# Kernel optimization log

Hardware: AMD Instinct MI355X
Metric: run time of the kernel (lower is better)

The kernel has to match this reference:

```python
import math
import jax, jax.numpy as jnp
import numpy as np

B, L, D, H, DFF, T, V = 512, 128, 128, 4, 256, 2048, 20000
LN_EPS = 1e-5
LOG_SIGMA0 = math.log(0.1)


def _keygen(base):
    c = [0]
    def nk():
        k = jax.random.fold_in(base, c[0]); c[0] += 1
        return k
    return nk


def bayes_linear(x, wmu, wls, bmu, bls, nk):
    # weight = mu + exp(log_sigma) * eps (fresh eps every call, as in BayesLinear.forward)
    w = wmu + jnp.exp(wls) * jax.random.normal(nk(), wmu.shape, wmu.dtype)
    b = bmu + jnp.exp(bls) * jax.random.normal(nk(), bmu.shape, bmu.dtype)
    return jnp.einsum('...d,od->...o', x, w) + b


def layer_norm(x, g, b):
    m = x.mean(-1, keepdims=True)
    v = ((x - m) ** 2).mean(-1, keepdims=True)
    return (x - m) / jnp.sqrt(v + LN_EPS) * g + b


def mha(q, k, v, wmu, wls, bmu, bls, nk):
    # wmu: [4, D, D] for q, k, v, o projections
    dk = D // H
    def proj(x, i):
        return bayes_linear(x, wmu[i], wls[i], bmu[i], bls[i], nk)
    def split(x):
        return x.reshape(B, L, H, dk).transpose(0, 2, 1, 3)
    Q, K, Vh = split(proj(q, 0)), split(proj(k, 1)), split(proj(v, 2))
    probs = jax.nn.softmax(jnp.einsum('bhqd,bhkd->bhqk', Q, K) / math.sqrt(dk), axis=-1)
    out = jnp.einsum('bhqk,bhkd->bhqd', probs, Vh).transpose(0, 2, 1, 3).reshape(B, L, D)
    return bayes_linear(out, wmu[3], wls[3], bmu[3], bls[3], nk)


def setup_inputs() -> dict:
    key = jax.random.key(0)
    ks = iter(jax.random.split(key, 64))
    def u(shape, fan_in):
        s = 1.0 / math.sqrt(fan_in)
        return jax.random.uniform(next(ks), shape, jnp.float32, -s, s)
    def ls(shape):
        return jnp.full(shape, LOG_SIGMA0, jnp.float32)
    return dict(
        event_set=jax.random.randint(next(ks), (B, L), 0, V),
        time=jax.random.uniform(next(ks), (B, L), jnp.float32),
        mask=jax.random.randint(next(ks), (B, L), 0, L),
        set_size=jax.random.randint(next(ks), (B,), 1, L),
        emb=jax.random.normal(next(ks), (V, D), jnp.float32),
        dec_wmu=u((2, 8, D, D), D), dec_wls=ls((2, 8, D, D)),
        dec_bmu=u((2, 8, D), D), dec_bls=ls((2, 8, D)),
        ffn1_wmu=u((2, DFF, D), D), ffn1_wls=ls((2, DFF, D)),
        ffn1_bmu=u((2, DFF), D), ffn1_bls=ls((2, DFF)),
        ffn2_wmu=u((2, D, DFF), DFF), ffn2_wls=ls((2, D, DFF)),
        ffn2_bmu=u((2, D), DFF), ffn2_bls=ls((2, D)),
        ln_g=jnp.ones((2, 3, D), jnp.float32), ln_b=jnp.zeros((2, 3, D), jnp.float32),
        alpha_wmu=u((5, T, D), D), alpha_wls=ls((5, T, D)),
        alpha_bmu=u((5, T), D), alpha_bls=ls((5, T)),
        at_wmu=u((5, 1, D), D), at_wls=ls((5, 1, D)),
        at_bmu=u((5, 1), D), at_bls=ls((5, 1)),
        em_w=u((5, T, D), D), em_b=u((5, T), D),
        es_w=u((5, T, D), D), es_b=u((5, T), D),
        tm_w=u((5, 1, D), D), tm_b=u((5, 1), D),
        ts_w=u((5, 1, D), D), ts_b=u((5, 1), D),
    )


def reference(event_set, time, mask, set_size, emb,
              dec_wmu, dec_wls, dec_bmu, dec_bls,
              ffn1_wmu, ffn1_wls, ffn1_bmu, ffn1_bls,
              ffn2_wmu, ffn2_wls, ffn2_bmu, ffn2_bls,
              ln_g, ln_b, alpha_wmu, alpha_wls, alpha_bmu, alpha_bls,
              at_wmu, at_wls, at_bmu, at_bls,
              em_w, em_b, es_w, es_b, tm_w, tm_b, ts_w, ts_b):
    nk = _keygen(jax.random.key(42))
    x = emb[event_set]                                     # [B, L, D]
    # sinusoidal positional encoding driven by `mask` (integer positions)
    pos = mask.astype(jnp.float32)
    div = jnp.exp(jnp.arange(D, dtype=jnp.float32) * (-math.log(10000.0) / D))
    ang = pos[..., None] * div                             # [B, L, D]
    pos_enc = jnp.where((mask % 2 == 0)[..., None], jnp.sin(ang), jnp.cos(ang))
    inp_x = x + pos_enc
    # two decoder layers: self-attn on x, cross-attn against inp_x (dropout = eval identity)
    for l in range(2):
        a = mha(x, x, x, dec_wmu[l, :4], dec_wls[l, :4], dec_bmu[l, :4], dec_bls[l, :4], nk)
        x = layer_norm(x + a, ln_g[l, 0], ln_b[l, 0])
        a = mha(x, inp_x, inp_x, dec_wmu[l, 4:], dec_wls[l, 4:], dec_bmu[l, 4:], dec_bls[l, 4:], nk)
        x = layer_norm(x + a, ln_g[l, 1], ln_b[l, 1])
        h1 = jax.nn.relu(bayes_linear(x, ffn1_wmu[l], ffn1_wls[l], ffn1_bmu[l], ffn1_bls[l], nk))
        f = bayes_linear(h1, ffn2_wmu[l], ffn2_wls[l], ffn2_bmu[l], ffn2_bls[l], nk)
        x = layer_norm(x + f, ln_g[l, 2], ln_b[l, 2])
    h = x[:, 0, :]                                          # [B, D]
    # 5 Bayesian alpha heads -> softmax over mixture dim (vectorized over k)
    aw = alpha_wmu + jnp.exp(alpha_wls) * jax.random.normal(nk(), alpha_wmu.shape)
    ab = alpha_bmu + jnp.exp(alpha_bls) * jax.random.normal(nk(), alpha_bmu.shape)
    alpha = jax.nn.softmax(jnp.einsum('bd,ktd->btk', h, aw) + ab.T[None], axis=2)   # [B, T, 5]
    atw = at_wmu + jnp.exp(at_wls) * jax.random.normal(nk(), at_wmu.shape)
    atb = at_bmu + jnp.exp(at_bls) * jax.random.normal(nk(), at_bmu.shape)
    alpha_t = jax.nn.softmax(jnp.einsum('bd,kd->bk', h, atw[:, 0]) + atb[:, 0][None], axis=1)  # [B, 5]
    # mixture of 5 reparameterized Gaussian predictors (plain Linears)
    means = jnp.einsum('bd,ktd->bkt', h, em_w) + em_b[None]          # [B, 5, T]
    stds = jnp.exp(jnp.einsum('bd,ktd->bkt', h, es_w) + es_b[None])
    noise_e = jax.random.normal(nk(), (B, 5, T))
    event_pred = jnp.sum(jnp.swapaxes(alpha, 1, 2) * (means + stds * noise_e), axis=1)   # [B, T]
    tmeans = jnp.einsum('bd,kd->bk', h, tm_w[:, 0]) + tm_b[:, 0][None]                   # [B, 5]
    tstds = jnp.exp(jnp.einsum('bd,kd->bk', h, ts_w[:, 0]) + ts_b[:, 0][None])
    noise_t = jax.random.normal(nk(), (B, 5))
    time_pred = jnp.sum(alpha_t * (tmeans + tstds * noise_t), axis=1, keepdims=True)     # [B, 1]
    return event_pred, time_pred
```

## Files before the change

### kernel.cpp

```cpp
#include <hip/hip_runtime.h>
#include <cstdint>
#include <cstddef>


#define NB   512
#define NL   128
#define ND   128
#define NH   4
#define NDFF 256
#define NT   2048
#define BL   (NB * NL)

typedef __attribute__((ext_vector_type(8))) short bf16x8;
typedef __attribute__((ext_vector_type(4))) float f32x4;

#define MFMA16(a, b, c) __builtin_amdgcn_mfma_f32_16x16x32_bf16((a), (b), (c), 0, 0, 0)

__host__ __device__ __forceinline__ void tf2x32(uint32_t k0, uint32_t k1,
                                                uint32_t x0, uint32_t x1,
                                                uint32_t& o0, uint32_t& o1)
{
  const uint32_t ks2 = k0 ^ k1 ^ 0x1BD11BDAu;
  x0 += k0; x1 += k1;
#define TF_RND(r) { x0 += x1; x1 = (x1 << (r)) | (x1 >> (32 - (r))); x1 ^= x0; }
  TF_RND(13) TF_RND(15) TF_RND(26) TF_RND(6)
  x0 += k1;  x1 += ks2 + 1u;
  TF_RND(17) TF_RND(29) TF_RND(16) TF_RND(24)
  x0 += ks2; x1 += k0 + 2u;
  TF_RND(13) TF_RND(15) TF_RND(26) TF_RND(6)
  x0 += k0;  x1 += k1 + 3u;
  TF_RND(17) TF_RND(29) TF_RND(16) TF_RND(24)
  x0 += k1;  x1 += ks2 + 4u;
  TF_RND(13) TF_RND(15) TF_RND(26) TF_RND(6)
  x0 += ks2; x1 += k0 + 5u;
#undef TF_RND
  o0 = x0; o1 = x1;
}

__device__ __forceinline__ float erfinv32(float x)
{
  float w = -log1pf(-__fmul_rn(x, x));
  float p;
  if (w < 5.0f) {
    w = w - 2.5f;
    p = 2.81022636e-08f;
    p = __fadd_rn( 3.43273939e-07f, __fmul_rn(p, w));
    p = __fadd_rn(-3.5233877e-06f,  __fmul_rn(p, w));
    p = __fadd_rn(-4.39150654e-06f, __fmul_rn(p, w));
    p = __fadd_rn( 0.00021858087f,  __fmul_rn(p, w));
    p = __fadd_rn(-0.00125372503f,  __fmul_rn(p, w));
    p = __fadd_rn(-0.00417768164f,  __fmul_rn(p, w));
    p = __fadd_rn( 0.246640727f,    __fmul_rn(p, w));
    p = __fadd_rn( 1.50140941f,     __fmul_rn(p, w));
  } else {
    w = sqrtf(w) - 3.0f;
    p = -0.000200214257f;
    p = __fadd_rn( 0.000100950558f, __fmul_rn(p, w));
    p = __fadd_rn( 0.00134934322f,  __fmul_rn(p, w));
    p = __fadd_rn(-0.00367342844f,  __fmul_rn(p, w));
    p = __fadd_rn( 0.00573950773f,  __fmul_rn(p, w));
    p = __fadd_rn(-0.0076224613f,   __fmul_rn(p, w));
    p = __fadd_rn( 0.00943887047f,  __fmul_rn(p, w));
    p = __fadd_rn( 1.00167406f,     __fmul_rn(p, w));
    p = __fadd_rn( 2.83297682f,     __fmul_rn(p, w));
  }
  return __fmul_rn(p, x);
}

__device__ __forceinline__ float bits_to_normal(uint32_t bits)
{
  const float lo = -0.99999994f;
  float f = __uint_as_float((bits >> 9) | 0x3F800000u) - 1.0f;
  float u = __fadd_rn(__fmul_rn(f, 2.0f), lo);
  u = fmaxf(lo, u);
  return __fmul_rn(1.41421356f, erfinv32(u));
}

__device__ __forceinline__ float jax_normal_idx(uint32_t k0, uint32_t k1, uint32_t idx)
{
  uint32_t o0, o1;
  tf2x32(k0, k1, 0u, idx, o0, o1);
  return bits_to_normal(o0 ^ o1);
}

__device__ __forceinline__ ushort f2bf(float f)
{
  uint32_t u = __float_as_uint(f);
  u += 0x7fffu + ((u >> 16) & 1u);
  return (ushort)(u >> 16);
}

__device__ __forceinline__ int pk128(int row, int col)
{
  return (((row >> 4) * 4 + (col >> 5)) * 64 + ((col >> 3) & 3) * 16 + (row & 15)) * 8
         + (col & 7);
}
__device__ __forceinline__ int pk_w2(int row, int col)
{
  return (col >> 7) * 16384 +
         (((row >> 4) * 4 + ((col >> 5) & 3)) * 64 + ((col >> 3) & 3) * 16 + (row & 15)) * 8
         + (col & 7);
}

#define SA_DECB 262144
#define SA_F1W  264192
#define SA_F1B  329728
#define SA_F2W  330240
#define SA_F2B  395776
#define SA_AW   396032
#define SA_AB   1706752
#define SA_ATW  1716992
#define SA_ATB  1717632
#define SA_TOT  1717637

#define BW_DEC  0
#define BW_F1   262144
#define BW_F2   327680
#define BW_AW   393216
#define BW_TOT  1703936

#define BF_DECB 0
#define BF_F1B  2048
#define BF_F2B  2560
#define BF_AB   2816
#define BF_ATW  13056
#define BF_ATB  13696
#define BF_TOT  13701

__global__ __launch_bounds__(256) void sample_all_kernel(
    const float* __restrict__ dec_wmu, const float* __restrict__ dec_wls,
    const float* __restrict__ dec_bmu, const float* __restrict__ dec_bls,
    const float* __restrict__ f1_wmu,  const float* __restrict__ f1_wls,
    const float* __restrict__ f1_bmu,  const float* __restrict__ f1_bls,
    const float* __restrict__ f2_wmu,  const float* __restrict__ f2_wls,
    const float* __restrict__ f2_bmu,  const float* __restrict__ f2_bls,
    const float* __restrict__ a_wmu,   const float* __restrict__ a_wls,
    const float* __restrict__ a_bmu,   const float* __restrict__ a_bls,
    const float* __restrict__ at_wmu,  const float* __restrict__ at_wls,
    const float* __restrict__ at_bmu,  const float* __restrict__ at_bls,
    ushort* __restrict__ wbf, float* __restrict__ wf32)
{
  const int i = blockIdx.x * 256 + threadIdx.x;
  if (i >= SA_TOT) return;
  const float* mu; const float* ls;
  uint32_t c, idx;
  int bf_dst = -1, f32_dst = -1;
  if (i < SA_DECB) {
    int s = i >> 14, t = i & 16383;
    mu = dec_wmu + i; ls = dec_wls + i;
    c = 2u * s + (s >= 8 ? 4u : 0u); idx = (uint32_t)t;
    bf_dst = BW_DEC + s * 16384 + pk128(t >> 7, t & 127);
  } else if (i < SA_F1W) {
    int t = i - SA_DECB; int s = t >> 7;
    mu = dec_bmu + t; ls = dec_bls + t;
    c = 2u * s + 1u + (s >= 8 ? 4u : 0u); idx = (uint32_t)(t & 127);
    f32_dst = BF_DECB + t;
  } else if (i < SA_F1B) {
    int t = i - SA_F1W; int s = t >> 15, tl = t & 32767;
    mu = f1_wmu + t; ls = f1_wls + t;
    c = 16u + 20u * s; idx = (uint32_t)tl;
    bf_dst = BW_F1 + s * 32768 + pk128(tl >> 7, tl & 127);
  } else if (i < SA_F2W) {
    int t = i - SA_F1B; int s = t >> 8;
    mu = f1_bmu + t; ls = f1_bls + t;
    c = 17u + 20u * s; idx = (uint32_t)(t & 255);
    f32_dst = BF_F1B + t;
  } else if (i < SA_F2B) {
    int t = i - SA_F2W; int s = t >> 15, tl = t & 32767;
    mu = f2_wmu + t; ls = f2_wls + t;
    c = 18u + 20u * s; idx = (uint32_t)tl;
    bf_dst = BW_F2 + s * 32768 + pk_w2(tl >> 8, tl & 255);
  } else if (i < SA_AW) {
    int t = i - SA_F2B; int s = t >> 7;
    mu = f2_bmu + t; ls = f2_bls + t;
    c = 19u + 20u * s; idx = (uint32_t)(t & 127);
    f32_dst = BF_F2B + t;
  } else if (i < SA_AB) {
    int t = i - SA_AW;
    mu = a_wmu + t; ls = a_wls + t; c = 40u; idx = (uint32_t)t;
    int kcomp = t >> 18, rem = t & 262143;
    bf_dst = BW_AW + pk128(kcomp * 2048 + (rem >> 7), rem & 127);
  } else if (i < SA_ATW) {
    int t = i - SA_AB;
    mu = a_bmu + t; ls = a_bls + t; c = 41u; idx = (uint32_t)t;
    f32_dst = BF_AB + t;
  } else if (i < SA_ATB) {
    int t = i - SA_ATW;
    mu = at_wmu + t; ls = at_wls + t; c = 42u; idx = (uint32_t)t;
    f32_dst = BF_ATW + t;
  } else {
    int t = i - SA_ATB;
    mu = at_bmu + t; ls = at_bls + t; c = 43u; idx = (uint32_t)t;
    f32_dst = BF_ATB + t;
  }
  uint32_t k0, k1;
  tf2x32(0u, 42u, 0u, c, k0, k1);
  float v = mu[0] + expf(ls[0]) * jax_normal_idx(k0, k1, idx);
  if (bf_dst >= 0) wbf[bf_dst] = f2bf(v);
  else             wf32[f32_dst] = v;
}

__global__ __launch_bounds__(256) void pack_head_kernel(
    const float* __restrict__ em_w, const float* __restrict__ es_w,
    ushort* __restrict__ EMp, ushort* __restrict__ ESp)
{
  int i = blockIdx.x * 256 + threadIdx.x;
  int kcomp = i >> 18, rem = i & 262143;
  int dst = pk128(kcomp * 2048 + (rem >> 7), rem & 127);
  EMp[dst] = f2bf(em_w[i]);
  ESp[dst] = f2bf(es_w[i]);
}

#define STR 136

__global__ __launch_bounds__(512, 1) void decoder_mega_kernel(
    const int* __restrict__ ev, const int* __restrict__ mask,
    const float* __restrict__ emb,
    const ushort* __restrict__ WBF, const float* __restrict__ WF32,
    const float* __restrict__ lng_all, const float* __restrict__ lnb_all,
    float* __restrict__ Xh, ushort* __restrict__ Hb)
{
  __shared__ ushort WL[16384];
  __shared__ ushort Kt[128][STR];
  __shared__ ushort Vt[128][STR];
  __shared__ ushort Xb[128][STR];

  const int b = blockIdx.x;
  const int tid = threadIdx.x;
  const int w = tid >> 6, l = tid & 63;
  const int g = l >> 4, r16 = l & 15;
  const f32x4 zero = {0.f, 0.f, 0.f, 0.f};
  ushort* KtLin = &Kt[0][0];

  auto stageW = [&](ushort* dst, const ushort* src) {
#pragma unroll
    for (int it = 0; it < 4; ++it) {
      __builtin_amdgcn_global_load_lds(
          (const uint32_t*)(src + (size_t)(it * 512 + tid) * 8),
          (uint32_t*)(dst + (it * 512 + w * 64) * 8), 16, 0, 0);
    }
  };
  auto wfrag = [&](const ushort* WB, int fid) -> bf16x8 {
    return *(const bf16x8*)(WB + (size_t)((fid << 6) + l) * 8);
  };

  float xreg[8][4];
  {
    int ecr[4];
#pragma unroll
    for (int r = 0; r < 4; ++r) ecr[r] = ev[b * NL + 16 * w + 4 * g + r];
#pragma unroll
    for (int c = 0; c < 8; ++c)
#pragma unroll
      for (int r = 0; r < 4; ++r) {
        float x = emb[(size_t)ecr[r] * ND + 16 * c + r16];
        xreg[c][r] = x;
        Xb[16 * w + 4 * g + r][16 * c + r16] = f2bf(x);
      }
  }
  bf16x8 inpx[4];
  {
    const int row = 16 * w + r16;
    const int ea = ev[b * NL + row];
    const int mk = mask[b * NL + row];
    const bool even = (mk & 1) == 0;
    const float fm = (float)mk;
#pragma unroll
    for (int ks = 0; ks < 4; ++ks) {
      float4 x0 = *(const float4*)(emb + (size_t)ea * ND + 32 * ks + 8 * g);
      float4 x1 = *(const float4*)(emb + (size_t)ea * ND + 32 * ks + 8 * g + 4);
      float xs[8] = {x0.x, x0.y, x0.z, x0.w, x1.x, x1.y, x1.z, x1.w};
      bf16x8 v;
#pragma unroll
      for (int e = 0; e < 8; ++e) {
        int d = 32 * ks + 8 * g + e;
        float div = expf((float)d * (float)(-9.210340371976184 / 128.0));
        float ang = fm * div;
        float pe = even ? sinf(ang) : cosf(ang);
        v[e] = (short)f2bf(xs[e] + pe);
      }
      inpx[ks] = v;
    }
  }

#pragma unroll 1
  for (int st = 0; st < 6; ++st) {
    const int lay = st / 3, m = st - 3 * lay;
    const float* lng = lng_all + (size_t)(lay * 3 + m) * ND;
    const float* lnb = lnb_all + (size_t)(lay * 3 + m) * ND;
    f32x4 acc2[8];
#pragma unroll
    for (int c = 0; c < 8; ++c) acc2[c] = zero;
    float bo[8];

    if (m < 2) {
      const int s0 = lay * 8 + m * 4;
      const ushort* W4 = WBF + BW_DEC + (size_t)s0 * 16384;
      const float*  B4 = WF32 + BF_DECB + (size_t)s0 * 128;

      __syncthreads();
      stageW(KtLin, W4 + 16384);
      stageW(WL,    W4 + 2 * 16384);
      __syncthreads();

      f32x4 kacc[8], vacc[8];
#pragma unroll
      for (int c = 0; c < 8; ++c) { kacc[c] = zero; vacc[c] = zero; }
#pragma unroll
      for (int ks = 0; ks < 4; ++ks) {
        bf16x8 a = (m == 0) ? *(const bf16x8*)&Xb[16 * w + r16][32 * ks + 8 * g]
                            : inpx[ks];
#pragma unroll
        for (int c = 0; c < 8; ++c) {
          kacc[c] = MFMA16(a, wfrag(KtLin, 4 * c + ks), kacc[c]);
          vacc[c] = MFMA16(a, wfrag(WL,    4 * c + ks), vacc[c]);
        }
      }
      __syncthreads();

#pragma unroll
      for (int c = 0; c < 8; ++c) {
        float kb = B4[128 + 16 * c + r16];
#pragma unroll
        for (int r = 0; r < 4; ++r)
          Kt[16 * w + 4 * g + r][16 * c + r16] = f2bf(kacc[c][r] + kb);
        float vb = B4[256 + 16 * c + r16];
        ushort4 pkv;
        pkv.x = f2bf(vacc[c][0] + vb); pkv.y = f2bf(vacc[c][1] + vb);
        pkv.z = f2bf(vacc[c][2] + vb); pkv.w = f2bf(vacc[c][3] + vb);
        *(ushort4*)&Vt[16 * c + r16][16 * w + 4 * g] = pkv;
      }
      stageW(WL, W4);
      __syncthreads();

      {
        f32x4 qacc[8];
#pragma unroll
        for (int c = 0; c < 8; ++c) qacc[c] = zero;
#pragma unroll
        for (int ks = 0; ks < 4; ++ks) {
          bf16x8 a = *(const bf16x8*)&Xb[16 * w + r16][32 * ks + 8 * g];
#pragma unroll
          for (int c = 0; c < 8; ++c)
            qacc[c] = MFMA16(a, wfrag(WL, 4 * c + ks), qacc[c]);
        }
#pragma unroll
        for (int c = 0; c < 8; ++c) {
          float qb = B4[16 * c + r16];
#pragma unroll
          for (int r = 0; r < 4; ++r)
            Xb[16 * w + 4 * g + r][16 * c + r16] = f2bf(qacc[c][r] + qb);
        }
      }
      __syncthreads();

      ushort (*Ps)[72] = (ushort(*)[72])WL;
      const float scale = 0.1767766952966369f;
      f32x4 oacc[4][2];
#pragma unroll
      for (int h = 0; h < 4; ++h) { oacc[h][0] = zero; oacc[h][1] = zero; }
#pragma unroll 1
      for (int h = 0; h < 4; ++h) {
        bf16x8 qa = *(const bf16x8*)&Xb[16 * w + r16][32 * h + 8 * g];
        f32x4 s[8];
#pragma unroll
        for (int c = 0; c < 8; ++c) {
          bf16x8 kv = *(const bf16x8*)&Kt[16 * c + r16][32 * h + 8 * g];
          s[c] = MFMA16(qa, kv, zero);
        }
        float pv[4][8];
#pragma unroll
        for (int r = 0; r < 4; ++r) {
          float v[8]; float mx = -1e30f;
#pragma unroll
          for (int c = 0; c < 8; ++c) { v[c] = s[c][r] * scale; mx = fmaxf(mx, v[c]); }
#pragma unroll
          for (int o = 1; o < 16; o <<= 1) mx = fmaxf(mx, __shfl_xor(mx, o));
          float sum = 0.f;
#pragma unroll
          for (int c = 0; c < 8; ++c) { v[c] = __expf(v[c] - mx); sum += v[c]; }
#pragma unroll
          for (int o = 1; o < 16; o <<= 1) sum += __shfl_xor(sum, o);
          float inv = 1.0f / sum;
#pragma unroll
          for (int c = 0; c < 8; ++c) pv[r][c] = v[c] * inv;
        }
#pragma unroll
        for (int kc = 0; kc < 4; ++kc) {
          const int po = (kc & 1) * 32;
#pragma unroll
          for (int c2 = 0; c2 < 2; ++c2)
#pragma unroll
            for (int r = 0; r < 4; ++r)
              Ps[16 * w + 4 * g + r][po + 16 * c2 + r16] = f2bf(pv[r][2 * kc + c2]);
          bf16x8 pa = *(const bf16x8*)&Ps[16 * w + r16][po + 8 * g];
#pragma unroll
          for (int cc = 0; cc < 2; ++cc) {
            bf16x8 vv = *(const bf16x8*)&Vt[32 * h + 16 * cc + r16][32 * kc + 8 * g];
            oacc[h][cc] = MFMA16(pa, vv, oacc[h][cc]);
          }
        }
      }
      __syncthreads();

#pragma unroll
      for (int h = 0; h < 4; ++h)
#pragma unroll
        for (int cc = 0; cc < 2; ++cc)
#pragma unroll
          for (int r = 0; r < 4; ++r)
            Kt[16 * w + 4 * g + r][32 * h + 16 * cc + r16] = f2bf(oacc[h][cc][r]);
      stageW(WL, W4 + 3 * 16384);
      __syncthreads();
#pragma unroll
      for (int ks = 0; ks < 4; ++ks) {
        bf16x8 a = *(const bf16x8*)&Kt[16 * w + r16][32 * ks + 8 * g];
#pragma unroll
        for (int c = 0; c < 8; ++c)
          acc2[c] = MFMA16(a, wfrag(WL, 4 * c + ks), acc2[c]);
      }
#pragma unroll
      for (int c = 0; c < 8; ++c) bo[c] = B4[384 + 16 * c + r16];
    } else {
      const ushort* W1p = WBF + BW_F1 + (size_t)lay * 32768;
      const ushort* W2p = WBF + BW_F2 + (size_t)lay * 32768;
      const float*  B1 = WF32 + BF_F1B + (size_t)lay * 256;
      const float*  B2 = WF32 + BF_F2B + (size_t)lay * 128;

      __syncthreads();
      stageW(WL,    W1p);
      stageW(KtLin, W1p + 16384);
      __syncthreads();

      f32x4 acc1[16];
#pragma unroll
      for (int c = 0; c < 16; ++c) acc1[c] = zero;
#pragma unroll
      for (int ks = 0; ks < 4; ++ks) {
        bf16x8 a = *(const bf16x8*)&Xb[16 * w + r16][32 * ks + 8 * g];
#pragma unroll
        for (int c = 0; c < 8; ++c) {
          acc1[c]     = MFMA16(a, wfrag(WL,    4 * c + ks), acc1[c]);
          acc1[8 + c] = MFMA16(a, wfrag(KtLin, 4 * c + ks), acc1[8 + c]);
        }
      }
      __syncthreads();

#pragma unroll
      for (int c = 0; c < 16; ++c) {
        float bb = B1[16 * c + r16];
#pragma unroll
        for (int r = 0; r < 4; ++r) {
          float o = fmaxf(acc1[c][r] + bb, 0.f);
          if (c < 8) Vt[16 * w + 4 * g + r][16 * c + r16] = f2bf(o);
          else       Kt[16 * w + 4 * g + r][16 * (c - 8) + r16] = f2bf(o);
        }
      }
      stageW(WL, W2p);
      __syncthreads();
#pragma unroll
      for (int kl = 0; kl < 4; ++kl) {
        bf16x8 a = *(const bf16x8*)&Vt[16 * w + r16][32 * kl + 8 * g];
#pragma unroll
        for (int c = 0; c < 8; ++c)
          acc2[c] = MFMA16(a, wfrag(WL, 4 * c + kl), acc2[c]);
      }
      __syncthreads();
      stageW(WL, W2p + 16384);
      __syncthreads();
#pragma unroll
      for (int kl = 0; kl < 4; ++kl) {
        bf16x8 a = *(const bf16x8*)&Kt[16 * w + r16][32 * kl + 8 * g];
#pragma unroll
        for (int c = 0; c < 8; ++c)
          acc2[c] = MFMA16(a, wfrag(WL, 4 * c + kl), acc2[c]);
      }
#pragma unroll
      for (int c = 0; c < 8; ++c) bo[c] = B2[16 * c + r16];
    }

    float gg[8], lb[8];
#pragma unroll
    for (int c = 0; c < 8; ++c) { gg[c] = lng[16 * c + r16]; lb[c] = lnb[16 * c + r16]; }
#pragma unroll
    for (int r = 0; r < 4; ++r) {
      float xv[8];
#pragma unroll
      for (int c = 0; c < 8; ++c) xv[c] = acc2[c][r] + bo[c] + xreg[c][r];
      float s = 0.f;
#pragma unroll
      for (int c = 0; c < 8; ++c) s += xv[c];
#pragma unroll
      for (int o = 1; o < 16; o <<= 1) s += __shfl_xor(s, o);
      float mean = s * (1.0f / 128.0f);
      float q = 0.f;
#pragma unroll
      for (int c = 0; c < 8; ++c) { float d = xv[c] - mean; q += d * d; }
#pragma unroll
      for (int o = 1; o < 16; o <<= 1) q += __shfl_xor(q, o);
      float inv = 1.0f / sqrtf(q * (1.0f / 128.0f) + 1e-5f);
#pragma unroll
      for (int c = 0; c < 8; ++c) {
        float o = (xv[c] - mean) * inv * gg[c] + lb[c];
        xreg[c][r] = o;
        Xb[16 * w + 4 * g + r][16 * c + r16] = f2bf(o);
      }
    }
  }

  if (w == 0 && g == 0) {
#pragma unroll
    for (int c = 0; c < 8; ++c) {
      Xh[(size_t)b * ND + 16 * c + r16] = xreg[c][0];
      Hb[(size_t)b * ND + 16 * c + r16] = f2bf(xreg[c][0]);
    }
  }
}

__global__ __launch_bounds__(256) void head_fused_kernel(
    const ushort* __restrict__ Hb,
    const ushort* __restrict__ AWp, const float* __restrict__ ABs,
    const ushort* __restrict__ EMp, const float* __restrict__ em_b,
    const ushort* __restrict__ ESp, const float* __restrict__ es_b,
    float* __restrict__ out, uint32_t k0, uint32_t k1)
{
  const int tt = blockIdx.x;
  const int t0 = tt * 16;
  const int bm = blockIdx.y * 128;
  const int tid = threadIdx.x;
  const int w = tid >> 6, l = tid & 63;
  const int g = l >> 4, r16 = l & 15;
  const f32x4 zero = {0.f, 0.f, 0.f, 0.f};
  const int tl = t0 + r16;

  f32x4 aA[2][5], aE[2][5], aS[2][5];
#pragma unroll
  for (int t = 0; t < 2; ++t)
#pragma unroll
    for (int k = 0; k < 5; ++k) { aA[t][k] = zero; aE[t][k] = zero; aS[t][k] = zero; }

#pragma unroll
  for (int ks = 0; ks < 4; ++ks) {
    bf16x8 a0 = *(const bf16x8*)(Hb + (size_t)(bm + 32 * w + r16) * 128 + 32 * ks + 8 * g);
    bf16x8 a1 = *(const bf16x8*)(Hb + (size_t)(bm + 32 * w + 16 + r16) * 128 + 32 * ks + 8 * g);
#pragma unroll
    for (int k = 0; k < 5; ++k) {
      const size_t CB = (((size_t)(k * 128 + tt) * 4 + ks) * 64 + l) * 8;
      bf16x8 wa = *(const bf16x8*)(AWp + CB);
      aA[0][k] = MFMA16(a0, wa, aA[0][k]);
      aA[1][k] = MFMA16(a1, wa, aA[1][k]);
      bf16x8 we = *(const bf16x8*)(EMp + CB);
      aE[0][k] = MFMA16(a0, we, aE[0][k]);
      aE[1][k] = MFMA16(a1, we, aE[1][k]);
      bf16x8 wsv = *(const bf16x8*)(ESp + CB);
      aS[0][k] = MFMA16(a0, wsv, aS[0][k]);
      aS[1][k] = MFMA16(a1, wsv, aS[1][k]);
    }
  }

  float bA[5], bE[5], bS[5];
#pragma unroll
  for (int k = 0; k < 5; ++k) {
    bA[k] = ABs[k * NT + tl];
    bE[k] = em_b[k * NT + tl];
    bS[k] = es_b[k * NT + tl];
  }

#pragma unroll
  for (int t = 0; t < 2; ++t)
#pragma unroll
    for (int r = 0; r < 4; ++r) {
      const int brow = bm + 32 * w + 16 * t + 4 * g + r;
      float lg[5];
      float mx = -1e30f;
#pragma unroll
      for (int k = 0; k < 5; ++k) { lg[k] = aA[t][k][r] + bA[k]; mx = fmaxf(mx, lg[k]); }
      float se = 0.f;
#pragma unroll
      for (int k = 0; k < 5; ++k) { lg[k] = expf(lg[k] - mx); se += lg[k]; }
      const float inv = 1.0f / se;
      float acc = 0.f;
#pragma unroll
      for (int k = 0; k < 5; ++k) {
        float nz = jax_normal_idx(k0, k1, (uint32_t)((brow * 5 + k) * NT + tl));
        float mean = aE[t][k][r] + bE[k];
        float sd   = expf(aS[t][k][r] + bS[k]);
        acc += (lg[k] * inv) * (mean + sd * nz);
      }
      out[(size_t)brow * NT + tl] = acc;
    }
}

__global__ __launch_bounds__(64) void time_head_kernel(
    const float* __restrict__ Xh, const float* __restrict__ atw,
    const float* __restrict__ atb, const float* __restrict__ tmw,
    const float* __restrict__ tmb, const float* __restrict__ tsw,
    const float* __restrict__ tsb, float* __restrict__ out,
    uint32_t k0, uint32_t k1)
{
  const int b = blockIdx.x;
  const int l = threadIdx.x;
  const float* h = Xh + (size_t)b * ND;
  const float h0 = h[l], h1 = h[l + 64];
  float lg[5], tm[5], tsl[5];
#pragma unroll
  for (int k = 0; k < 5; ++k) {
    float s0 = fmaf(h0, atw[k * ND + l], h1 * atw[k * ND + l + 64]);
    float s1 = fmaf(h0, tmw[k * ND + l], h1 * tmw[k * ND + l + 64]);
    float s2 = fmaf(h0, tsw[k * ND + l], h1 * tsw[k * ND + l + 64]);
#pragma unroll
    for (int o = 32; o; o >>= 1) {
      s0 += __shfl_xor(s0, o);
      s1 += __shfl_xor(s1, o);
      s2 += __shfl_xor(s2, o);
    }
    lg[k] = s0 + atb[k]; tm[k] = s1 + tmb[k]; tsl[k] = s2 + tsb[k];
  }
  if (l == 0) {
    float mx = lg[0];
    for (int k = 1; k < 5; ++k) mx = fmaxf(mx, lg[k]);
    float se = 0.f;
    for (int k = 0; k < 5; ++k) { lg[k] = expf(lg[k] - mx); se += lg[k]; }
    float acc = 0.f;
    for (int k = 0; k < 5; ++k) {
      float nz = jax_normal_idx(k0, k1, (uint32_t)(b * 5 + k));
      acc += (lg[k] / se) * (tm[k] + expf(tsl[k]) * nz);
    }
    out[b] = acc;
  }
}

extern "C" void kernel_launch(void* const* d_in, const int* in_sizes, int n_in,
                              void* d_out, int out_size, void* d_ws, size_t ws_size,
                              hipStream_t stream)
{
  (void)in_sizes; (void)n_in; (void)out_size; (void)ws_size;

  const int*   ev      = (const int*)d_in[0];
  const int*   mask    = (const int*)d_in[2];
  const float* emb     = (const float*)d_in[4];
  const float* dec_wmu = (const float*)d_in[5];
  const float* dec_wls = (const float*)d_in[6];
  const float* dec_bmu = (const float*)d_in[7];
  const float* dec_bls = (const float*)d_in[8];
  const float* f1_wmu  = (const float*)d_in[9];
  const float* f1_wls  = (const float*)d_in[10];
  const float* f1_bmu  = (const float*)d_in[11];
  const float* f1_bls  = (const float*)d_in[12];
  const float* f2_wmu  = (const float*)d_in[13];
  const float* f2_wls  = (const float*)d_in[14];
  const float* f2_bmu  = (const float*)d_in[15];
  const float* f2_bls  = (const float*)d_in[16];
  const float* ln_g    = (const float*)d_in[17];
  const float* ln_b    = (const float*)d_in[18];
  const float* a_wmu   = (const float*)d_in[19];
  const float* a_wls   = (const float*)d_in[20];
  const float* a_bmu   = (const float*)d_in[21];
  const float* a_bls   = (const float*)d_in[22];
  const float* at_wmu  = (const float*)d_in[23];
  const float* at_wls  = (const float*)d_in[24];
  const float* at_bmu  = (const float*)d_in[25];
  const float* at_bls  = (const float*)d_in[26];
  const float* em_w    = (const float*)d_in[27];
  const float* em_b    = (const float*)d_in[28];
  const float* es_w    = (const float*)d_in[29];
  const float* es_b    = (const float*)d_in[30];
  const float* tm_w    = (const float*)d_in[31];
  const float* tm_b    = (const float*)d_in[32];
  const float* ts_w    = (const float*)d_in[33];
  const float* ts_b    = (const float*)d_in[34];

  float* ws = (float*)d_ws;
  ushort* WBF  = (ushort*)ws;
  float*  WF32 = ws + BW_TOT / 2;
  ushort* EMp  = (ushort*)(WF32 + BF_TOT + 3);
  ushort* ESp  = EMp + 5 * NT * ND;
  ushort* Hb   = ESp + 5 * NT * ND;
  float*  Xh   = (float*)(Hb + (size_t)NB * ND);

  uint32_t fk0[46], fk1[46];
  for (uint32_t c = 0; c < 46; ++c) tf2x32(0u, 42u, 0u, c, fk0[c], fk1[c]);

  sample_all_kernel<<<dim3((SA_TOT + 255) / 256), dim3(256), 0, stream>>>(
      dec_wmu, dec_wls, dec_bmu, dec_bls,
      f1_wmu, f1_wls, f1_bmu, f1_bls,
      f2_wmu, f2_wls, f2_bmu, f2_bls,
      a_wmu, a_wls, a_bmu, a_bls,
      at_wmu, at_wls, at_bmu, at_bls, WBF, WF32);

  pack_head_kernel<<<dim3((5 * NT * ND) / 256), dim3(256), 0, stream>>>(
      em_w, es_w, EMp, ESp);

  decoder_mega_kernel<<<dim3(NB), dim3(512), 0, stream>>>(
      ev, mask, emb, WBF, WF32, ln_g, ln_b, Xh, Hb);

  float* out = (float*)d_out;
  head_fused_kernel<<<dim3(NT / 16, 4), dim3(256), 0, stream>>>(
      Hb, WBF + BW_AW, WF32 + BF_AB, EMp, em_b, ESp, es_b,
      out, fk0[44], fk1[44]);
  time_head_kernel<<<dim3(NB), dim3(64), 0, stream>>>(
      Xh, WF32 + BF_ATW, WF32 + BF_ATB, tm_w, tm_b, ts_w, ts_b,
      out + (size_t)NB * NT, fk0[45], fk1[45]);
}
```

Measured before the change: 328.6 us.

## Read weight fragments directly from global memory instead of staging into LDS

Drops the LDS weight buffer and the async global-to-LDS staging of each 128x128 weight matrix. MFMA B-fragments are now loaded straight from global memory, which is expected to be served mostly from L2. The Q projection is fused into the K/V projection loop, and many __syncthreads barriers tied to staging are removed. The intent is to cut barrier stalls and serialized staging phases, at the cost of each wave fetching the full weights on its own, raising L2 traffic and exposing global-load latency right next to the MFMAs.

Result: slower. 583.5 us (+77.6%).

```diff
diff --git a/kernel.cpp b/kernel.cpp
--- a/kernel.cpp
+++ b/kernel.cpp
@@ -220,28 +220,19 @@
     const float* __restrict__ lng_all, const float* __restrict__ lnb_all,
     float* __restrict__ Xh, ushort* __restrict__ Hb)
 {
-  __shared__ ushort WL[16384];
   __shared__ ushort Kt[128][STR];
   __shared__ ushort Vt[128][STR];
   __shared__ ushort Xb[128][STR];
+  __shared__ ushort Ps[128][72];
 
   const int b = blockIdx.x;
   const int tid = threadIdx.x;
   const int w = tid >> 6, l = tid & 63;
   const int g = l >> 4, r16 = l & 15;
   const f32x4 zero = {0.f, 0.f, 0.f, 0.f};
-  ushort* KtLin = &Kt[0][0];
-
-  auto stageW = [&](ushort* dst, const ushort* src) {
-#pragma unroll
-    for (int it = 0; it < 4; ++it) {
-      __builtin_amdgcn_global_load_lds(
-          (const uint32_t*)(src + (size_t)(it * 512 + tid) * 8),
-          (uint32_t*)(dst + (it * 512 + w * 64) * 8), 16, 0, 0);
-    }
-  };
-  auto wfrag = [&](const ushort* WB, int fid) -> bf16x8 {
-    return *(const bf16x8*)(WB + (size_t)((fid << 6) + l) * 8);
+
+  auto wfragG = [&](const ushort* Wp, int fid) -> bf16x8 {
+    return *(const bf16x8*)(Wp + ((size_t)(fid << 6) + l) * 8);
   };
 
   float xreg[8][4];
@@ -295,25 +286,24 @@
 
     if (m < 2) {
       const int s0 = lay * 8 + m * 4;
-      const ushort* W4 = WBF + BW_DEC + (size_t)s0 * 16384;
+      const ushort* Wq = WBF + BW_DEC + (size_t)s0 * 16384;
+      const ushort* Wk = Wq + 16384;
+      const ushort* Wv = Wq + 2 * 16384;
+      const ushort* Wo = Wq + 3 * 16384;
       const float*  B4 = WF32 + BF_DECB + (size_t)s0 * 128;
 
-      __syncthreads();
-      stageW(KtLin, W4 + 16384);
-      stageW(WL,    W4 + 2 * 16384);
-      __syncthreads();
-
-      f32x4 kacc[8], vacc[8];
-#pragma unroll
-      for (int c = 0; c < 8; ++c) { kacc[c] = zero; vacc[c] = zero; }
+      f32x4 qacc[8], kacc[8], vacc[8];
+#pragma unroll
+      for (int c = 0; c < 8; ++c) { qacc[c] = zero; kacc[c] = zero; vacc[c] = zero; }
 #pragma unroll
       for (int ks = 0; ks < 4; ++ks) {
-        bf16x8 a = (m == 0) ? *(const bf16x8*)&Xb[16 * w + r16][32 * ks + 8 * g]
-                            : inpx[ks];
+        bf16x8 ax = *(const bf16x8*)&Xb[16 * w + r16][32 * ks + 8 * g];
+        bf16x8 akv = (m == 0) ? ax : inpx[ks];
 #pragma unroll
         for (int c = 0; c < 8; ++c) {
-          kacc[c] = MFMA16(a, wfrag(KtLin, 4 * c + ks), kacc[c]);
-          vacc[c] = MFMA16(a, wfrag(WL,    4 * c + ks), vacc[c]);
+          qacc[c] = MFMA16(ax,  wfragG(Wq, 4 * c + ks), qacc[c]);
+          kacc[c] = MFMA16(akv, wfragG(Wk, 4 * c + ks), kacc[c]);
+          vacc[c] = MFMA16(akv, wfragG(Wv, 4 * c + ks), vacc[c]);
         }
       }
       __syncthreads();
@@ -329,32 +319,13 @@
         pkv.x = f2bf(vacc[c][0] + vb); pkv.y = f2bf(vacc[c][1] + vb);
         pkv.z = f2bf(vacc[c][2] + vb); pkv.w = f2bf(vacc[c][3] + vb);
         *(ushort4*)&Vt[16 * c + r16][16 * w + 4 * g] = pkv;
-      }
-      stageW(WL, W4);
+        float qb = B4[16 * c + r16];
+#pragma unroll
+        for (int r = 0; r < 4; ++r)
+          Xb[16 * w + 4 * g + r][16 * c + r16] = f2bf(qacc[c][r] + qb);
+      }
       __syncthreads();
 
-      {
-        f32x4 qacc[8];
-#pragma unroll
-        for (int c = 0; c < 8; ++c) qacc[c] = zero;
-#pragma unroll
-        for (int ks = 0; ks < 4; ++ks) {
-          bf16x8 a = *(const bf16x8*)&Xb[16 * w + r16][32 * ks + 8 * g];
-#pragma unroll
-          for (int c = 0; c < 8; ++c)
-            qacc[c] = MFMA16(a, wfrag(WL, 4 * c + ks), qacc[c]);
-        }
-#pragma unroll
-        for (int c = 0; c < 8; ++c) {
-          float qb = B4[16 * c + r16];
-#pragma unroll
-          for (int r = 0; r < 4; ++r)
-            Xb[16 * w + 4 * g + r][16 * c + r16] = f2bf(qacc[c][r] + qb);
-        }
-      }
-      __syncthreads();
-
-      ushort (*Ps)[72] = (ushort(*)[72])WL;
       const float scale = 0.1767766952966369f;
       f32x4 oacc[4][2];
 #pragma unroll
@@ -410,14 +381,12 @@
 #pragma unroll
           for (int r = 0; r < 4; ++r)
             Kt[16 * w + 4 * g + r][32 * h + 16 * cc + r16] = f2bf(oacc[h][cc][r]);
-      stageW(WL, W4 + 3 * 16384);
-      __syncthreads();
 #pragma unroll
       for (int ks = 0; ks < 4; ++ks) {
         bf16x8 a = *(const bf16x8*)&Kt[16 * w + r16][32 * ks + 8 * g];
 #pragma unroll
         for (int c = 0; c < 8; ++c)
-          acc2[c] = MFMA16(a, wfrag(WL, 4 * c + ks), acc2[c]);
+          acc2[c] = MFMA16(a, wfragG(Wo, 4 * c + ks), acc2[c]);
       }
 #pragma unroll
       for (int c = 0; c < 8; ++c) bo[c] = B4[384 + 16 * c + r16];
@@ -427,11 +396,6 @@
       const float*  B1 = WF32 + BF_F1B + (size_t)lay * 256;
       const float*  B2 = WF32 + BF_F2B + (size_t)lay * 128;
 
-      __syncthreads();
-      stageW(WL,    W1p);
-      stageW(KtLin, W1p + 16384);
-      __syncthreads();
-
       f32x4 acc1[16];
 #pragma unroll
       for (int c = 0; c < 16; ++c) acc1[c] = zero;
@@ -440,12 +404,10 @@
         bf16x8 a = *(const bf16x8*)&Xb[16 * w + r16][32 * ks + 8 * g];
 #pragma unroll
         for (int c = 0; c < 8; ++c) {
-          acc1[c]     = MFMA16(a, wfrag(WL,    4 * c + ks), acc1[c]);
-          acc1[8 + c] = MFMA16(a, wfrag(KtLin, 4 * c + ks), acc1[8 + c]);
+          acc1[c]     = MFMA16(a, wfragG(W1p,         4 * c + ks), acc1[c]);
+          acc1[8 + c] = MFMA16(a, wfragG(W1p + 16384, 4 * c + ks), acc1[8 + c]);
         }
       }
-      __syncthreads();
-
 #pragma unroll
       for (int c = 0; c < 16; ++c) {
         float bb = B1[16 * c + r16];
@@ -456,24 +418,19 @@
           else       Kt[16 * w + 4 * g + r][16 * (c - 8) + r16] = f2bf(o);
         }
       }
-      stageW(WL, W2p);
-      __syncthreads();
 #pragma unroll
       for (int kl = 0; kl < 4; ++kl) {
         bf16x8 a = *(const bf16x8*)&Vt[16 * w + r16][32 * kl + 8 * g];
 #pragma unroll
         for (int c = 0; c < 8; ++c)
-          acc2[c] = MFMA16(a, wfrag(WL, 4 * c + kl), acc2[c]);
-      }
-      __syncthreads();
-      stageW(WL, W2p + 16384);
-      __syncthreads();
+          acc2[c] = MFMA16(a, wfragG(W2p, 4 * c + kl), acc2[c]);
+      }
 #pragma unroll
       for (int kl = 0; kl < 4; ++kl) {
         bf16x8 a = *(const bf16x8*)&Kt[16 * w + r16][32 * kl + 8 * g];
 #pragma unroll
         for (int c = 0; c < 8; ++c)
-          acc2[c] = MFMA16(a, wfrag(WL, 4 * c + kl), acc2[c]);
+          acc2[c] = MFMA16(a, wfragG(W2p + 16384, 4 * c + kl), acc2[c]);
       }
 #pragma unroll
       for (int c = 0; c < 8; ++c) bo[c] = B2[16 * c + r16];
```

## Double-buffer decoder weight staging and swizzle LDS activation tiles

Applied to the files above, without the earlier changes.

The decoder megakernel gains a second LDS weight buffer. Each weight matrix's async global-to-LDS load is issued one GEMM ahead, including the first weight of the next sublayer, so weight fetches overlap with MFMA work instead of sitting between barriers. The padded activation tiles (stride 136) are replaced by unpadded 128-wide tiles with an XOR chunk swizzle to avoid bank conflicts. The head loop is also fully unrolled. LDS use grows, and the prefetch ordering relies on barriers that clear before the buffers are reused.

Result: slower. 343.8 us (+4.6%).

```diff
diff --git a/kernel.cpp b/kernel.cpp
--- a/kernel.cpp
+++ b/kernel.cpp
@@ -100,6 +100,15 @@
   return (col >> 7) * 16384 +
          (((row >> 4) * 4 + ((col >> 5) & 3)) * 64 + ((col >> 3) & 3) * 16 + (row & 15)) * 8
          + (col & 7);
+}
+
+__device__ __forceinline__ int swzc(int row, int chunk)
+{
+  return row * 128 + ((chunk ^ (row & 15)) << 3);
+}
+__device__ __forceinline__ int swz(int row, int col)
+{
+  return row * 128 + ((((col >> 3) ^ (row & 15)) << 3) | (col & 7));
 }
 
 #define SA_DECB 262144
@@ -211,8 +220,6 @@
   ESp[dst] = f2bf(es_w[i]);
 }
 
-#define STR 136
-
 __global__ __launch_bounds__(512, 1) void decoder_mega_kernel(
     const int* __restrict__ ev, const int* __restrict__ mask,
     const float* __restrict__ emb,
@@ -220,17 +227,17 @@
     const float* __restrict__ lng_all, const float* __restrict__ lnb_all,
     float* __restrict__ Xh, ushort* __restrict__ Hb)
 {
-  __shared__ ushort WL[16384];
-  __shared__ ushort Kt[128][STR];
-  __shared__ ushort Vt[128][STR];
-  __shared__ ushort Xb[128][STR];
+  __shared__ ushort WAu[16384];
+  __shared__ ushort WBu[16384];
+  __shared__ ushort KtU[16384];
+  __shared__ ushort VtU[16384];
+  __shared__ ushort XbU[16384];
 
   const int b = blockIdx.x;
   const int tid = threadIdx.x;
   const int w = tid >> 6, l = tid & 63;
   const int g = l >> 4, r16 = l & 15;
   const f32x4 zero = {0.f, 0.f, 0.f, 0.f};
-  ushort* KtLin = &Kt[0][0];
 
   auto stageW = [&](ushort* dst, const ushort* src) {
 #pragma unroll
@@ -240,9 +247,19 @@
           (uint32_t*)(dst + (it * 512 + w * 64) * 8), 16, 0, 0);
     }
   };
-  auto wfrag = [&](const ushort* WB, int fid) -> bf16x8 {
-    return *(const bf16x8*)(WB + (size_t)((fid << 6) + l) * 8);
+  auto wfrag = [&](const ushort* WBp, int fid) -> bf16x8 {
+    return *(const bf16x8*)(WBp + (size_t)((fid << 6) + l) * 8);
   };
+
+  const ushort* firstW[6];
+  firstW[0] = WBF + BW_DEC + (size_t)1 * 16384;
+  firstW[1] = WBF + BW_DEC + (size_t)5 * 16384;
+  firstW[2] = WBF + BW_F1;
+  firstW[3] = WBF + BW_DEC + (size_t)9 * 16384;
+  firstW[4] = WBF + BW_DEC + (size_t)13 * 16384;
+  firstW[5] = WBF + BW_F1 + 32768;
+
+  stageW(WAu, firstW[0]);
 
   float xreg[8][4];
   {
@@ -255,7 +272,7 @@
       for (int r = 0; r < 4; ++r) {
         float x = emb[(size_t)ecr[r] * ND + 16 * c + r16];
         xreg[c][r] = x;
-        Xb[16 * w + 4 * g + r][16 * c + r16] = f2bf(x);
+        XbU[swz(16 * w + 4 * g + r, 16 * c + r16)] = f2bf(x);
       }
   }
   bf16x8 inpx[4];
@@ -295,77 +312,91 @@
 
     if (m < 2) {
       const int s0 = lay * 8 + m * 4;
-      const ushort* W4 = WBF + BW_DEC + (size_t)s0 * 16384;
+      const ushort* Wq = WBF + BW_DEC + (size_t)(s0 + 0) * 16384;
+      const ushort* Wv = WBF + BW_DEC + (size_t)(s0 + 2) * 16384;
+      const ushort* Wo = WBF + BW_DEC + (size_t)(s0 + 3) * 16384;
       const float*  B4 = WF32 + BF_DECB + (size_t)s0 * 128;
 
       __syncthreads();
-      stageW(KtLin, W4 + 16384);
-      stageW(WL,    W4 + 2 * 16384);
-      __syncthreads();
-
-      f32x4 kacc[8], vacc[8];
-#pragma unroll
-      for (int c = 0; c < 8; ++c) { kacc[c] = zero; vacc[c] = zero; }
+      stageW(WBu, Wv);
+      f32x4 kacc[8];
+#pragma unroll
+      for (int c = 0; c < 8; ++c) kacc[c] = zero;
 #pragma unroll
       for (int ks = 0; ks < 4; ++ks) {
-        bf16x8 a = (m == 0) ? *(const bf16x8*)&Xb[16 * w + r16][32 * ks + 8 * g]
+        bf16x8 a = (m == 0) ? *(const bf16x8*)&XbU[swzc(16 * w + r16, 4 * ks + g)]
                             : inpx[ks];
 #pragma unroll
-        for (int c = 0; c < 8; ++c) {
-          kacc[c] = MFMA16(a, wfrag(KtLin, 4 * c + ks), kacc[c]);
-          vacc[c] = MFMA16(a, wfrag(WL,    4 * c + ks), vacc[c]);
-        }
-      }
-      __syncthreads();
-
+        for (int c = 0; c < 8; ++c)
+          kacc[c] = MFMA16(a, wfrag(WAu, 4 * c + ks), kacc[c]);
+      }
+
+      __syncthreads();
+      stageW(WAu, Wq);
 #pragma unroll
       for (int c = 0; c < 8; ++c) {
         float kb = B4[128 + 16 * c + r16];
 #pragma unroll
         for (int r = 0; r < 4; ++r)
-          Kt[16 * w + 4 * g + r][16 * c + r16] = f2bf(kacc[c][r] + kb);
-        float vb = B4[256 + 16 * c + r16];
-        ushort4 pkv;
-        pkv.x = f2bf(vacc[c][0] + vb); pkv.y = f2bf(vacc[c][1] + vb);
-        pkv.z = f2bf(vacc[c][2] + vb); pkv.w = f2bf(vacc[c][3] + vb);
-        *(ushort4*)&Vt[16 * c + r16][16 * w + 4 * g] = pkv;
-      }
-      stageW(WL, W4);
-      __syncthreads();
-
+          KtU[swz(16 * w + 4 * g + r, 16 * c + r16)] = f2bf(kacc[c][r] + kb);
+      }
+      {
+        f32x4 vacc[8];
+#pragma unroll
+        for (int c = 0; c < 8; ++c) vacc[c] = zero;
+#pragma unroll
+        for (int ks = 0; ks < 4; ++ks) {
+          bf16x8 a = (m == 0) ? *(const bf16x8*)&XbU[swzc(16 * w + r16, 4 * ks + g)]
+                              : inpx[ks];
+#pragma unroll
+          for (int c = 0; c < 8; ++c)
+            vacc[c] = MFMA16(a, wfrag(WBu, 4 * c + ks), vacc[c]);
+        }
+#pragma unroll
+        for (int c = 0; c < 8; ++c) {
+          float vb = B4[256 + 16 * c + r16];
+          ushort4 pkv;
+          pkv.x = f2bf(vacc[c][0] + vb); pkv.y = f2bf(vacc[c][1] + vb);
+          pkv.z = f2bf(vacc[c][2] + vb); pkv.w = f2bf(vacc[c][3] + vb);
+          *(ushort4*)&VtU[swzc(16 * c + r16, 2 * w + (g >> 1)) + (g & 1) * 4] = pkv;
+        }
+      }
+
+      __syncthreads();
+      stageW(WBu, Wo);
       {
         f32x4 qacc[8];
 #pragma unroll
         for (int c = 0; c < 8; ++c) qacc[c] = zero;
 #pragma unroll
         for (int ks = 0; ks < 4; ++ks) {
-          bf16x8 a = *(const bf16x8*)&Xb[16 * w + r16][32 * ks + 8 * g];
+          bf16x8 a = *(const bf16x8*)&XbU[swzc(16 * w + r16, 4 * ks + g)];
 #pragma unroll
           for (int c = 0; c < 8; ++c)
-            qacc[c] = MFMA16(a, wfrag(WL, 4 * c + ks), qacc[c]);
+            qacc[c] = MFMA16(a, wfrag(WAu, 4 * c + ks), qacc[c]);
         }
 #pragma unroll
         for (int c = 0; c < 8; ++c) {
           float qb = B4[16 * c + r16];
 #pragma unroll
           for (int r = 0; r < 4; ++r)
-            Xb[16 * w + 4 * g + r][16 * c + r16] = f2bf(qacc[c][r] + qb);
-        }
-      }
-      __syncthreads();
-
-      ushort (*Ps)[72] = (ushort(*)[72])WL;
+            XbU[swz(16 * w + 4 * g + r, 16 * c + r16)] = f2bf(qacc[c][r] + qb);
+        }
+      }
+
+      __syncthreads();
+      ushort (*Ps)[72] = (ushort(*)[72])WAu;
       const float scale = 0.1767766952966369f;
       f32x4 oacc[4][2];
 #pragma unroll
       for (int h = 0; h < 4; ++h) { oacc[h][0] = zero; oacc[h][1] = zero; }
-#pragma unroll 1
+#pragma unroll
       for (int h = 0; h < 4; ++h) {
-        bf16x8 qa = *(const bf16x8*)&Xb[16 * w + r16][32 * h + 8 * g];
+        bf16x8 qa = *(const bf16x8*)&XbU[swzc(16 * w + r16, 4 * h + g)];
         f32x4 s[8];
 #pragma unroll
         for (int c = 0; c < 8; ++c) {
-          bf16x8 kv = *(const bf16x8*)&Kt[16 * c + r16][32 * h + 8 * g];
+          bf16x8 kv = *(const bf16x8*)&KtU[swzc(16 * c + r16, 4 * h + g)];
           s[c] = MFMA16(qa, kv, zero);
         }
         float pv[4][8];
@@ -396,28 +427,27 @@
           bf16x8 pa = *(const bf16x8*)&Ps[16 * w + r16][po + 8 * g];
 #pragma unroll
           for (int cc = 0; cc < 2; ++cc) {
-            bf16x8 vv = *(const bf16x8*)&Vt[32 * h + 16 * cc + r16][32 * kc + 8 * g];
+            bf16x8 vv = *(const bf16x8*)&VtU[swzc(32 * h + 16 * cc + r16, 4 * kc + g)];
             oacc[h][cc] = MFMA16(pa, vv, oacc[h][cc]);
           }
         }
       }
-      __syncthreads();
-
+
+      __syncthreads();
+      if (st < 5) stageW(WAu, firstW[st + 1]);
 #pragma unroll
       for (int h = 0; h < 4; ++h)
 #pragma unroll
         for (int cc = 0; cc < 2; ++cc)
 #pragma unroll
           for (int r = 0; r < 4; ++r)
-            Kt[16 * w + 4 * g + r][32 * h + 16 * cc + r16] = f2bf(oacc[h][cc][r]);
-      stageW(WL, W4 + 3 * 16384);
-      __syncthreads();
+            KtU[swz(16 * w + 4 * g + r, 32 * h + 16 * cc + r16)] = f2bf(oacc[h][cc][r]);
 #pragma unroll
       for (int ks = 0; ks < 4; ++ks) {
-        bf16x8 a = *(const bf16x8*)&Kt[16 * w + r16][32 * ks + 8 * g];
+        bf16x8 a = *(const bf16x8*)&KtU[swzc(16 * w + r16, 4 * ks + g)];
 #pragma unroll
         for (int c = 0; c < 8; ++c)
-          acc2[c] = MFMA16(a, wfrag(WL, 4 * c + ks), acc2[c]);
+          acc2[c] = MFMA16(a, wfrag(WBu, 4 * c + ks), acc2[c]);
       }
 #pragma unroll
       for (int c = 0; c < 8; ++c) bo[c] = B4[384 + 16 * c + r16];
@@ -428,52 +458,64 @@
       const float*  B2 = WF32 + BF_F2B + (size_t)lay * 128;
 
       __syncthreads();
-      stageW(WL,    W1p);
-      stageW(KtLin, W1p + 16384);
-      __syncthreads();
-
-      f32x4 acc1[16];
-#pragma unroll
-      for (int c = 0; c < 16; ++c) acc1[c] = zero;
+      stageW(WBu, W1p + 16384);
+      f32x4 acc1a[8];
+#pragma unroll
+      for (int c = 0; c < 8; ++c) acc1a[c] = zero;
 #pragma unroll
       for (int ks = 0; ks < 4; ++ks) {
-        bf16x8 a = *(const bf16x8*)&Xb[16 * w + r16][32 * ks + 8 * g];
+        bf16x8 a = *(const bf16x8*)&XbU[swzc(16 * w + r16, 4 * ks + g)];
+#pragma unroll
+        for (int c = 0; c < 8; ++c)
+          acc1a[c] = MFMA16(a, wfrag(WAu, 4 * c + ks), acc1a[c]);
+      }
+
+      __syncthreads();
+      stageW(WAu, W2p);
+      {
+        f32x4 acc1b[8];
+#pragma unroll
+        for (int c = 0; c < 8; ++c) acc1b[c] = zero;
+#pragma unroll
+        for (int ks = 0; ks < 4; ++ks) {
+          bf16x8 a = *(const bf16x8*)&XbU[swzc(16 * w + r16, 4 * ks + g)];
+#pragma unroll
+          for (int c = 0; c < 8; ++c)
+            acc1b[c] = MFMA16(a, wfrag(WBu, 4 * c + ks), acc1b[c]);
+        }
 #pragma unroll
         for (int c = 0; c < 8; ++c) {
-          acc1[c]     = MFMA16(a, wfrag(WL,    4 * c + ks), acc1[c]);
-          acc1[8 + c] = MFMA16(a, wfrag(KtLin, 4 * c + ks), acc1[8 + c]);
-        }
-      }
-      __syncthreads();
-
-#pragma unroll
-      for (int c = 0; c < 16; ++c) {
-        float bb = B1[16 * c + r16];
-#pragma unroll
-        for (int r = 0; r < 4; ++r) {
-          float o = fmaxf(acc1[c][r] + bb, 0.f);
-          if (c < 8) Vt[16 * w + 4 * g + r][16 * c + r16] = f2bf(o);
-          else       Kt[16 * w + 4 * g + r][16 * (c - 8) + r16] = f2bf(o);
-        }
-      }
-      stageW(WL, W2p);
-      __syncthreads();
+          float b1a = B1[16 * c + r16];
+#pragma unroll
+          for (int r = 0; r < 4; ++r)
+            VtU[swz(16 * w + 4 * g + r, 16 * c + r16)] =
+                f2bf(fmaxf(acc1a[c][r] + b1a, 0.f));
+          float b1b = B1[128 + 16 * c + r16];
+#pragma unroll
+          for (int r = 0; r < 4; ++r)
+            KtU[swz(16 * w + 4 * g + r, 16 * c + r16)] =
+                f2bf(fmaxf(acc1b[c][r] + b1b, 0.f));
+        }
+      }
+
+      __syncthreads();
+      stageW(WBu, W2p + 16384);
 #pragma unroll
       for (int kl = 0; kl < 4; ++kl) {
-        bf16x8 a = *(const bf16x8*)&Vt[16 * w + r16][32 * kl + 8 * g];
+        bf16x8 a = *(const bf16x8*)&VtU[swzc(16 * w + r16, 4 * kl + g)];
 #pragma unroll
         for (int c = 0; c < 8; ++c)
-          acc2[c] = MFMA16(a, wfrag(WL, 4 * c + kl), acc2[c]);
-      }
-      __syncthreads();
-      stageW(WL, W2p + 16384);
-      __syncthreads();
+          acc2[c] = MFMA16(a, wfrag(WAu, 4 * c + kl), acc2[c]);
+      }
+
+      __syncthreads();
+      if (st < 5) stageW(WAu, firstW[st + 1]);
 #pragma unroll
       for (int kl = 0; kl < 4; ++kl) {
-        bf16x8 a = *(const bf16x8*)&Kt[16 * w + r16][32 * kl + 8 * g];
+        bf16x8 a = *(const bf16x8*)&KtU[swzc(16 * w + r16, 4 * kl + g)];
 #pragma unroll
         for (int c = 0; c < 8; ++c)
-          acc2[c] = MFMA16(a, wfrag(WL, 4 * c + kl), acc2[c]);
+          acc2[c] = MFMA16(a, wfrag(WBu, 4 * c + kl), acc2[c]);
       }
 #pragma unroll
       for (int c = 0; c < 8; ++c) bo[c] = B2[16 * c + r16];
@@ -503,7 +545,7 @@
       for (int c = 0; c < 8; ++c) {
         float o = (xv[c] - mean) * inv * gg[c] + lb[c];
         xreg[c][r] = o;
-        Xb[16 * w + 4 * g + r][16 * c + r16] = f2bf(o);
+        XbU[swz(16 * w + 4 * g + r, 16 * c + r16)] = f2bf(o);
       }
     }
   }
```
